# Kernel tuning notes

Measured on AMD Instinct MI355X. Metric: run time of the kernel, lower is better.

## Reference

```python
import jax, jax.numpy as jnp
import numpy as np

H, C = 8, 32          # heads, per-head channels (h_feats)
NEG_SLOPE = 0.2


def setup_inputs() -> dict:
    key = jax.random.key(0)
    ks = jax.random.split(key, 9)
    N, E, F_IN, F_E = 50000, 800000, 128, 16
    x = jax.random.normal(ks[0], (N, F_IN), jnp.float32)
    edge_index = jax.random.randint(ks[1], (2, E), 0, N, jnp.int64)
    edge_attr = jax.random.normal(ks[2], (E, F_E), jnp.float32)
    s = 1.0 / np.sqrt(F_IN)
    W = jax.random.normal(ks[3], (H * C, F_IN), jnp.float32) * s
    W_edge = jax.random.normal(ks[4], (H * C, F_E), jnp.float32) * (1.0 / np.sqrt(F_E))
    att_src = jax.random.normal(ks[5], (H, C), jnp.float32) * (1.0 / np.sqrt(C))
    att_dst = jax.random.normal(ks[6], (H, C), jnp.float32) * (1.0 / np.sqrt(C))
    att_edge = jax.random.normal(ks[7], (H, C), jnp.float32) * (1.0 / np.sqrt(C))
    bias = jnp.zeros((C,), jnp.float32)
    return {"x": x, "edge_index": edge_index, "edge_attr": edge_attr,
            "W": W, "W_edge": W_edge, "att_src": att_src, "att_dst": att_dst,
            "att_edge": att_edge, "bias": bias}


def reference(x, edge_index, edge_attr, W, W_edge, att_src, att_dst, att_edge, bias):
    N = x.shape[0]
    src, dst = edge_index[0], edge_index[1]

    # --- add self loops, edge_attr fill_value='mean' (per-dst mean of incoming attrs) ---
    deg = jax.ops.segment_sum(jnp.ones_like(dst, dtype=edge_attr.dtype), dst, num_segments=N)
    loop_attr = jax.ops.segment_sum(edge_attr, dst, num_segments=N) / jnp.maximum(deg, 1.0)[:, None]
    loop = jnp.arange(N, dtype=src.dtype)
    src = jnp.concatenate([src, loop])
    dst = jnp.concatenate([dst, loop])
    ea = jnp.concatenate([edge_attr, loop_attr], axis=0)  # [E+N, F_e]

    # --- node projection and per-node attention terms ---
    xh = (x @ W.T).reshape(N, H, C)                      # [N,H,C]
    a_src = jnp.einsum('nhc,hc->nh', xh, att_src)        # [N,H]
    a_dst = jnp.einsum('nhc,hc->nh', xh, att_dst)        # [N,H]

    # edge attention folded: (lin_edge(e).view(E,H,C) * att_edge).sum(-1) == e @ M
    M = jnp.einsum('hcf,hc->fh', W_edge.reshape(H, C, -1), att_edge)  # [F_e,H]
    a_edge = ea @ M                                      # [E+N,H]

    alpha = a_src[src] + a_dst[dst] + a_edge             # [E+N,H]
    alpha = jnp.where(alpha >= 0, alpha, NEG_SLOPE * alpha)

    # --- scatter-softmax over edges grouped by dst node ---
    amax = jax.ops.segment_max(alpha, dst, num_segments=N)  # every node has a self loop
    ex = jnp.exp(alpha - amax[dst])
    denom = jax.ops.segment_sum(ex, dst, num_segments=N)
    att = ex / denom[dst]                                # [E+N,H]

    # --- weighted message scatter-sum ---
    msg = xh[src] * att[..., None]                       # [E+N,H,C]
    out = jax.ops.segment_sum(msg, dst, num_segments=N)  # [N,H,C]
    return out.mean(axis=1) + bias                       # concat=False -> head mean
```

## Files before the change

### kernel.cpp

```cpp
#include <hip/hip_runtime.h>
#include <math.h>

#define H 8
#define C 32
#define HC 256
#define FE 16
#define FIN 128
#define NEG_SLOPE 0.2f

typedef __attribute__((ext_vector_type(8))) short bf16x8;
typedef __attribute__((ext_vector_type(4))) float f32x4;

__device__ __forceinline__ unsigned short f2bf(float f) {
  unsigned int u = __float_as_uint(f);
  unsigned int lsb = (u >> 16) & 1u;
  u += 0x7fffu + lsb;
  return (unsigned short)(u >> 16);
}
__device__ __forceinline__ float bf2f(unsigned short s) {
  return __uint_as_float(((unsigned int)s) << 16);
}

__device__ __forceinline__ void split8(const float* v, bf16x8& hi, bf16x8& lo) {
#pragma unroll
  for (int i = 0; i < 8; ++i) {
    unsigned int u = __float_as_uint(v[i]);
    unsigned int hu = u & 0xffff0000u;
    float r = v[i] - __uint_as_float(hu);
    hi[i] = (short)(hu >> 16);
    lo[i] = (short)f2bf(r);
  }
}

__global__ __launch_bounds__(256) void k_wsplit(const float* __restrict__ W,
                                                unsigned short* __restrict__ Whi,
                                                unsigned short* __restrict__ Wlo) {
  int i = blockIdx.x * 256 + threadIdx.x;
  float v = W[i];
  unsigned int u = __float_as_uint(v);
  unsigned int hu = u & 0xffff0000u;
  Whi[i] = (unsigned short)(hu >> 16);
  Wlo[i] = f2bf(v - __uint_as_float(hu)) , (unsigned short)0;
}

__global__ __launch_bounds__(256) void k_wsplit2(const float* __restrict__ W,
                                                 unsigned short* __restrict__ Whi,
                                                 unsigned short* __restrict__ Wlo) {
  int i = blockIdx.x * 256 + threadIdx.x;
  float v = W[i];
  unsigned int u = __float_as_uint(v);
  unsigned int hu = u & 0xffff0000u;
  Whi[i] = (unsigned short)(hu >> 16);
  Wlo[i] = f2bf(v - __uint_as_float(hu));
}

__global__ __launch_bounds__(256) void k_xh(const float* __restrict__ x,
                                            const unsigned short* __restrict__ Whi,
                                            const unsigned short* __restrict__ Wlo,
                                            const float* __restrict__ att_src,
                                            const float* __restrict__ att_dst,
                                            unsigned short* __restrict__ xhb,
                                            float* __restrict__ a_src,
                                            float* __restrict__ a_dst, int N) {
  int t = threadIdx.x;
  int w = t >> 6, lane = t & 63;
  int n15 = lane & 15, q = lane >> 4;
  int nodeBase = blockIdx.x * 128 + w * 32;
  int chBase = blockIdx.y * 128;

  f32x4 acc[8][2];
#pragma unroll
  for (int mt = 0; mt < 8; ++mt)
#pragma unroll
    for (int nt = 0; nt < 2; ++nt) acc[mt][nt] = (f32x4)(0.f);

  for (int ks = 0; ks < 4; ++ks) {
    int kOff = ks * 32 + q * 8;
    bf16x8 Bhi[2], Blo[2];
#pragma unroll
    for (int nt = 0; nt < 2; ++nt) {
      int node = nodeBase + nt * 16 + n15;
      int rn = (node < N) ? node : (N - 1);
      const float* px = &x[(size_t)rn * FIN + kOff];
      float vb[8];
      *(float4*)&vb[0] = *(const float4*)px;
      *(float4*)&vb[4] = *(const float4*)(px + 4);
      split8(vb, Bhi[nt], Blo[nt]);
    }
#pragma unroll
    for (int mt = 0; mt < 8; ++mt) {
      int widx = ((chBase + mt * 16 + n15) << 7) + kOff;
      bf16x8 Ahi = *(const bf16x8*)&Whi[widx];
      bf16x8 Alo = *(const bf16x8*)&Wlo[widx];
#pragma unroll
      for (int nt = 0; nt < 2; ++nt) {
        acc[mt][nt] = __builtin_amdgcn_mfma_f32_16x16x32_bf16(Ahi, Bhi[nt], acc[mt][nt], 0, 0, 0);
        acc[mt][nt] = __builtin_amdgcn_mfma_f32_16x16x32_bf16(Ahi, Blo[nt], acc[mt][nt], 0, 0, 0);
        acc[mt][nt] = __builtin_amdgcn_mfma_f32_16x16x32_bf16(Alo, Bhi[nt], acc[mt][nt], 0, 0, 0);
      }
    }
  }

  float ps[2][4] = {{0.f,0.f,0.f,0.f},{0.f,0.f,0.f,0.f}};
  float pd[2][4] = {{0.f,0.f,0.f,0.f},{0.f,0.f,0.f,0.f}};
#pragma unroll
  for (int mt = 0; mt < 8; ++mt) {
    int hl = mt >> 1;
#pragma unroll
    for (int r = 0; r < 4; ++r) {
      int ch = chBase + mt * 16 + q * 4 + r;
      float as_c = att_src[ch], ad_c = att_dst[ch];
#pragma unroll
      for (int nt = 0; nt < 2; ++nt) {
        float val = acc[mt][nt][r];
        ps[nt][hl] = fmaf(val, as_c, ps[nt][hl]);
        pd[nt][hl] = fmaf(val, ad_c, pd[nt][hl]);
      }
    }
#pragma unroll
    for (int nt = 0; nt < 2; ++nt) {
      int node = nodeBase + nt * 16 + n15;
      if (node < N) {
        ushort4 us;
        us.x = f2bf(acc[mt][nt][0]); us.y = f2bf(acc[mt][nt][1]);
        us.z = f2bf(acc[mt][nt][2]); us.w = f2bf(acc[mt][nt][3]);
        *(ushort4*)&xhb[(size_t)node * HC + chBase + mt * 16 + q * 4] = us;
      }
    }
  }
#pragma unroll
  for (int nt = 0; nt < 2; ++nt)
#pragma unroll
    for (int hl = 0; hl < 4; ++hl) {
      ps[nt][hl] += __shfl_xor(ps[nt][hl], 16, 64);
      ps[nt][hl] += __shfl_xor(ps[nt][hl], 32, 64);
      pd[nt][hl] += __shfl_xor(pd[nt][hl], 16, 64);
      pd[nt][hl] += __shfl_xor(pd[nt][hl], 32, 64);
    }
  if (q == 0) {
#pragma unroll
    for (int nt = 0; nt < 2; ++nt) {
      int node = nodeBase + nt * 16 + n15;
      if (node < N) {
        *(float4*)&a_src[node * H + blockIdx.y * 4] = make_float4(ps[nt][0], ps[nt][1], ps[nt][2], ps[nt][3]);
        *(float4*)&a_dst[node * H + blockIdx.y * 4] = make_float4(pd[nt][0], pd[nt][1], pd[nt][2], pd[nt][3]);
      }
    }
  }
}

__global__ __launch_bounds__(256) void k_deg(const int* __restrict__ ei,
                                             int* __restrict__ deg,
                                             int* __restrict__ rank, int E) {
  int e = blockIdx.x * 256 + threadIdx.x;
  if (e < E) rank[e] = atomicAdd(&deg[ei[E + e]], 1);
}

__global__ __launch_bounds__(256) void k_scan1(const int* __restrict__ deg,
                                               int* __restrict__ bsum, int N) {
  int t = threadIdx.x;
  int i = blockIdx.x * 256 + t;
  int v = (i < N) ? deg[i] : 0;
#pragma unroll
  for (int m = 1; m < 64; m <<= 1) v += __shfl_xor(v, m, 64);
  __shared__ int wsum[4];
  if ((t & 63) == 0) wsum[t >> 6] = v;
  __syncthreads();
  if (t == 0) bsum[blockIdx.x] = wsum[0] + wsum[1] + wsum[2] + wsum[3];
}

__global__ __launch_bounds__(256) void k_scan2(const int* __restrict__ bsum,
                                               int* __restrict__ boff, int nb) {
  __shared__ int buf[256];
  int t = threadIdx.x;
  int v = (t < nb) ? bsum[t] : 0;
  buf[t] = v;
  __syncthreads();
  for (int off = 1; off < 256; off <<= 1) {
    int y = (t >= off) ? buf[t - off] : 0;
    __syncthreads();
    buf[t] += y;
    __syncthreads();
  }
  if (t < nb) boff[t] = buf[t] - v;
}

__global__ __launch_bounds__(256) void k_scan3(const int* __restrict__ deg,
                                               const int* __restrict__ boff,
                                               int* __restrict__ rowptr, int N, int E) {
  __shared__ int buf[256];
  int t = threadIdx.x;
  int i = blockIdx.x * 256 + t;
  int v = (i < N) ? deg[i] : 0;
  buf[t] = v;
  __syncthreads();
  for (int off = 1; off < 256; off <<= 1) {
    int y = (t >= off) ? buf[t - off] : 0;
    __syncthreads();
    buf[t] += y;
    __syncthreads();
  }
  if (i < N) rowptr[i] = boff[blockIdx.x] + buf[t] - v;
  if (i == 0) rowptr[N] = E;
}

__global__ __launch_bounds__(256) void k_edge_scatter(const int* __restrict__ ei,
                                                      const float* __restrict__ ea,
                                                      const float* __restrict__ W_edge,
                                                      const float* __restrict__ att_edge,
                                                      const int* __restrict__ rowptr,
                                                      const int* __restrict__ rank,
                                                      unsigned short* __restrict__ recs, int E) {
  __shared__ float Ms[FE * H];
  int t = threadIdx.x;
  if (t < FE * H) {
    int f = t >> 3, h = t & 7;
    float acc = 0.f;
#pragma unroll
    for (int c = 0; c < C; ++c)
      acc += W_edge[(h * C + c) * FE + f] * att_edge[h * C + c];
    Ms[f * H + h] = acc;
  }
  __syncthreads();
  int e = blockIdx.x * 256 + t;
  if (e >= E) return;
  int s = ei[e], d = ei[E + e];
  const float4* p = (const float4*)&ea[(size_t)e * FE];
  float4 v0 = p[0], v1 = p[1], v2 = p[2], v3 = p[3];
  float eav[FE] = {v0.x, v0.y, v0.z, v0.w, v1.x, v1.y, v1.z, v1.w,
                   v2.x, v2.y, v2.z, v2.w, v3.x, v3.y, v3.z, v3.w};
  float o[H];
#pragma unroll
  for (int h = 0; h < H; ++h) {
    float acc = 0.f;
#pragma unroll
    for (int f = 0; f < FE; ++f) acc += eav[f] * Ms[f * H + h];
    o[h] = acc;
  }
  int pos = rowptr[d] + rank[e];
  uint4 pk;
  pk.x = (unsigned int)f2bf(o[0]) | ((unsigned int)f2bf(o[1]) << 16);
  pk.y = (unsigned int)f2bf(o[2]) | ((unsigned int)f2bf(o[3]) << 16);
  pk.z = (unsigned int)f2bf(o[4]) | ((unsigned int)f2bf(o[5]) << 16);
  pk.w = (unsigned int)f2bf(o[6]) | ((unsigned int)f2bf(o[7]) << 16);
  uint4 hv; hv.x = (unsigned int)s; hv.y = 0; hv.z = 0; hv.w = 0;
  unsigned short* rp = &recs[(size_t)pos * 16];
  *(uint4*)rp = pk;
  *(uint4*)(rp + 8) = hv;
}

__global__ __launch_bounds__(256) void k_node(const unsigned short* __restrict__ xhb,
                                              const float* __restrict__ a_src,
                                              const float* __restrict__ a_dst,
                                              const unsigned short* __restrict__ recs,
                                              const int* __restrict__ rowptr,
                                              const float* __restrict__ bias,
                                              float* __restrict__ out, int N) {
  __shared__ float wlds[4][512];
  __shared__ int   slds[4][64];
  int wv = threadIdx.x >> 6;
  int lane = threadIdx.x & 63;
  int n = blockIdx.x * 4 + wv;
  if (n >= N) return;
  int start = rowptr[n];
  int deg = rowptr[n + 1] - start;
  int h = lane & 7, esub = lane >> 3;
  float adst = a_dst[n * H + h];
  float asrc = a_src[n * H + h];

  float pmax = -1e30f, psum = 0.f;
  float a0, a1, a2, a3, a4, a5, a6, a7;
#define PH1(IT, AV)                                                          \
  {                                                                          \
    int j = IT * 8 + esub;                                                   \
    float al = -1e30f;                                                       \
    if (j < deg) {                                                           \
      int b = (start + j) * 16;                                              \
      float ae = bf2f(recs[b + h]);                                          \
      int src = *(const int*)&recs[b + 8];                                   \
      if (h == 0) slds[wv][j] = src;                                         \
      psum += ae;                                                            \
      al = a_src[src * H + h] + adst + ae;                                   \
      al = (al >= 0.f) ? al : NEG_SLOPE * al;                                \
      pmax = fmaxf(pmax, al);                                                \
    }                                                                        \
    AV = al;                                                                 \
  }
  PH1(0, a0) PH1(1, a1) PH1(2, a2) PH1(3, a3)
  PH1(4, a4) PH1(5, a5) PH1(6, a6) PH1(7, a7)
#undef PH1
  for (int j0 = 64; j0 < deg; j0 += 8) {
    int j = j0 + esub;
    if (j < deg) {
      int b = (start + j) * 16;
      float ae = bf2f(recs[b + h]);
      int src = *(const int*)&recs[b + 8];
      psum += ae;
      float al = a_src[src * H + h] + adst + ae;
      al = (al >= 0.f) ? al : NEG_SLOPE * al;
      pmax = fmaxf(pmax, al);
    }
  }
#pragma unroll
  for (int m = 8; m <= 32; m <<= 1) {
    pmax = fmaxf(pmax, __shfl_xor(pmax, m, 64));
    psum += __shfl_xor(psum, m, 64);
  }
  float aself = asrc + adst + psum / fmaxf((float)deg, 1.f);
  aself = (aself >= 0.f) ? aself : NEG_SLOPE * aself;
  float amax = fmaxf(pmax, aself);

  float den = 0.f;
#define PH2(IT, AV)                                                          \
  {                                                                          \
    int j = IT * 8 + esub;                                                   \
    if (j < deg) {                                                           \
      float wj = __expf(AV - amax);                                          \
      den += wj;                                                             \
      wlds[wv][j * 8 + h] = wj;                                              \
    }                                                                        \
  }
  PH2(0, a0) PH2(1, a1) PH2(2, a2) PH2(3, a3)
  PH2(4, a4) PH2(5, a5) PH2(6, a6) PH2(7, a7)
#undef PH2
  for (int j0 = 64; j0 < deg; j0 += 8) {
    int j = j0 + esub;
    if (j < deg) {
      int b = (start + j) * 16;
      float ae = bf2f(recs[b + h]);
      int src = *(const int*)&recs[b + 8];
      float al = a_src[src * H + h] + adst + ae;
      al = (al >= 0.f) ? al : NEG_SLOPE * al;
      den += __expf(al - amax);
    }
  }
#pragma unroll
  for (int m = 8; m <= 32; m <<= 1) den += __shfl_xor(den, m, 64);
  float wself = __expf(aself - amax);
  float inv = 1.f / (den + wself);

  int hc = lane >> 3;
  float inv_c  = __shfl(inv, hc, 64);
  float ws_c   = __shfl(wself, hc, 64);
  float amax_c = __shfl(amax, hc, 64);
  float adst_c = __shfl(adst, hc, 64);
  float accx, accy, accz, accw;
  {
    const uint2* px = (const uint2*)(xhb + (((unsigned)n) << 8));
    uint2 u = px[lane];
    accx = ws_c * __uint_as_float(u.x << 16);
    accy = ws_c * __uint_as_float(u.x & 0xffff0000u);
    accz = ws_c * __uint_as_float(u.y << 16);
    accw = ws_c * __uint_as_float(u.y & 0xffff0000u);
  }
  int dlim = (deg < 64) ? deg : 64;
#pragma unroll 2
  for (int j = 0; j < dlim; ++j) {
    float wj = wlds[wv][j * 8 + hc];
    int src = slds[wv][j];
    const uint2* p = (const uint2*)(xhb + (((unsigned)src) << 8));
    uint2 v = p[lane];
    accx = fmaf(__uint_as_float(v.x << 16), wj, accx);
    accy = fmaf(__uint_as_float(v.x & 0xffff0000u), wj, accy);
    accz = fmaf(__uint_as_float(v.y << 16), wj, accz);
    accw = fmaf(__uint_as_float(v.y & 0xffff0000u), wj, accw);
  }
  for (int j = 64; j < deg; ++j) {
    int b = (start + j) * 16;
    float ae = bf2f(recs[b + hc]);
    int src = *(const int*)&recs[b + 8];
    float al = a_src[src * H + hc] + adst_c + ae;
    al = (al >= 0.f) ? al : NEG_SLOPE * al;
    float wj = __expf(al - amax_c);
    const uint2* p = (const uint2*)(xhb + (((unsigned)src) << 8));
    uint2 v = p[lane];
    accx = fmaf(__uint_as_float(v.x << 16), wj, accx);
    accy = fmaf(__uint_as_float(v.x & 0xffff0000u), wj, accy);
    accz = fmaf(__uint_as_float(v.y << 16), wj, accz);
    accw = fmaf(__uint_as_float(v.y & 0xffff0000u), wj, accw);
  }
  accx *= inv_c; accy *= inv_c; accz *= inv_c; accw *= inv_c;

#pragma unroll
  for (int m = 8; m <= 32; m <<= 1) {
    accx += __shfl_xor(accx, m, 64);
    accy += __shfl_xor(accy, m, 64);
    accz += __shfl_xor(accz, m, 64);
    accw += __shfl_xor(accw, m, 64);
  }
  if (lane < 8) {
    float4 b = ((const float4*)bias)[lane];
    float4 o;
    o.x = accx * 0.125f + b.x;
    o.y = accy * 0.125f + b.y;
    o.z = accz * 0.125f + b.z;
    o.w = accw * 0.125f + b.w;
    ((float4*)&out[(size_t)n * C])[lane] = o;
  }
}

extern "C" void kernel_launch(void* const* d_in, const int* in_sizes, int n_in,
                              void* d_out, int out_size, void* d_ws, size_t ws_size,
                              hipStream_t stream) {
  const float* x        = (const float*)d_in[0];
  const int*   ei       = (const int*)d_in[1];
  const float* ea       = (const float*)d_in[2];
  const float* W        = (const float*)d_in[3];
  const float* W_edge   = (const float*)d_in[4];
  const float* att_src  = (const float*)d_in[5];
  const float* att_dst  = (const float*)d_in[6];
  const float* att_edge = (const float*)d_in[7];
  const float* bias     = (const float*)d_in[8];
  float* out = (float*)d_out;

  int N = in_sizes[0] / FIN;
  int E = in_sizes[1] / 2;
  int nb = (N + 255) / 256;

  char* ws = (char*)d_ws;
  auto take = [&](size_t bytes) {
    char* p = ws;
    ws += (bytes + 255) & ~(size_t)255;
    return p;
  };
  unsigned short* xhb    = (unsigned short*)take((size_t)N * HC * 2);
  float*          a_src  = (float*)take((size_t)N * H * 4);
  float*          a_dst  = (float*)take((size_t)N * H * 4);
  unsigned short* recs   = (unsigned short*)take((size_t)E * 32);
  unsigned short* Whi    = (unsigned short*)take((size_t)HC * FIN * 2);
  unsigned short* Wlo    = (unsigned short*)take((size_t)HC * FIN * 2);
  int*            deg    = (int*)take((size_t)N * 4);
  int*            rowptr = (int*)take((size_t)(N + 1) * 4);
  int*            rank   = (int*)take((size_t)E * 4);
  int*            bsum   = (int*)take((size_t)nb * 4);
  int*            boff   = (int*)take((size_t)nb * 4);

  hipMemsetAsync(deg, 0, (size_t)N * 4, stream);
  k_wsplit2<<<(HC * FIN) / 256, 256, 0, stream>>>(W, Whi, Wlo);
  k_deg<<<(E + 255) / 256, 256, 0, stream>>>(ei, deg, rank, E);
  k_xh<<<dim3((N + 127) / 128, 2), 256, 0, stream>>>(x, Whi, Wlo, att_src, att_dst, xhb, a_src, a_dst, N);
  k_scan1<<<nb, 256, 0, stream>>>(deg, bsum, N);
  k_scan2<<<1, 256, 0, stream>>>(bsum, boff, nb);
  k_scan3<<<nb, 256, 0, stream>>>(deg, boff, rowptr, N, E);
  k_edge_scatter<<<(E + 255) / 256, 256, 0, stream>>>(ei, ea, W_edge, att_edge, rowptr, rank, recs, E);
  k_node<<<(N + 3) / 4, 256, 0, stream>>>(xhb, a_src, a_dst, recs, rowptr, bias, out, N);
}
```

Baseline: 307.0 us.

## Batch edge gathers in k_node and fold W split into k_deg

The per-node kernel now issues all record loads for the first 64 edges up front, then all a_src gathers, before doing the softmax maths. The weighted-sum loop is software-pipelined so that eight neighbour feature rows are prefetched while the previous eight are accumulated. This is meant to raise memory-level parallelism and hide gather latency. The separate W hi/lo split kernel is merged into the degree-count kernel to save one launch, at the cost of more registers in k_node.

```diff
diff --git a/kernel.cpp b/kernel.cpp
--- a/kernel.cpp
+++ b/kernel.cpp
@@ -30,28 +30,6 @@
     hi[i] = (short)(hu >> 16);
     lo[i] = (short)f2bf(r);
   }
-}
-
-__global__ __launch_bounds__(256) void k_wsplit(const float* __restrict__ W,
-                                                unsigned short* __restrict__ Whi,
-                                                unsigned short* __restrict__ Wlo) {
-  int i = blockIdx.x * 256 + threadIdx.x;
-  float v = W[i];
-  unsigned int u = __float_as_uint(v);
-  unsigned int hu = u & 0xffff0000u;
-  Whi[i] = (unsigned short)(hu >> 16);
-  Wlo[i] = f2bf(v - __uint_as_float(hu)) , (unsigned short)0;
-}
-
-__global__ __launch_bounds__(256) void k_wsplit2(const float* __restrict__ W,
-                                                 unsigned short* __restrict__ Whi,
-                                                 unsigned short* __restrict__ Wlo) {
-  int i = blockIdx.x * 256 + threadIdx.x;
-  float v = W[i];
-  unsigned int u = __float_as_uint(v);
-  unsigned int hu = u & 0xffff0000u;
-  Whi[i] = (unsigned short)(hu >> 16);
-  Wlo[i] = f2bf(v - __uint_as_float(hu));
 }
 
 __global__ __launch_bounds__(256) void k_xh(const float* __restrict__ x,
@@ -151,8 +129,18 @@
 
 __global__ __launch_bounds__(256) void k_deg(const int* __restrict__ ei,
                                              int* __restrict__ deg,
-                                             int* __restrict__ rank, int E) {
+                                             int* __restrict__ rank,
+                                             const float* __restrict__ W,
+                                             unsigned short* __restrict__ Whi,
+                                             unsigned short* __restrict__ Wlo, int E) {
   int e = blockIdx.x * 256 + threadIdx.x;
+  if (e < HC * FIN) {
+    float v = W[e];
+    unsigned int u = __float_as_uint(v);
+    unsigned int hu = u & 0xffff0000u;
+    Whi[e] = (unsigned short)(hu >> 16);
+    Wlo[e] = f2bf(v - __uint_as_float(hu));
+  }
   if (e < E) rank[e] = atomicAdd(&deg[ei[E + e]], 1);
 }
 
@@ -264,41 +252,59 @@
   if (n >= N) return;
   int start = rowptr[n];
   int deg = rowptr[n + 1] - start;
+  int jmax = (deg < 64) ? deg : 64;
   int h = lane & 7, esub = lane >> 3;
   float adst = a_dst[n * H + h];
   float asrc = a_src[n * H + h];
 
+  float ae[8]; int sr[8];
+#pragma unroll
+  for (int it = 0; it < 8; ++it) {
+    int j = it * 8 + esub;
+    ae[it] = 0.f; sr[it] = 0;
+    if (j < jmax) {
+      const unsigned short* rp = &recs[(size_t)(start + j) * 16];
+      ae[it] = bf2f(rp[h]);
+      sr[it] = *(const int*)(rp + 8);
+    }
+  }
+  float asg[8];
+#pragma unroll
+  for (int it = 0; it < 8; ++it) {
+    int j = it * 8 + esub;
+    asg[it] = (j < jmax) ? a_src[sr[it] * H + h] : 0.f;
+  }
+  if (h == 0) {
+#pragma unroll
+    for (int it = 0; it < 8; ++it) {
+      int j = it * 8 + esub;
+      if (j < jmax) slds[wv][j] = sr[it];
+    }
+  }
+  float al[8];
   float pmax = -1e30f, psum = 0.f;
-  float a0, a1, a2, a3, a4, a5, a6, a7;
-#define PH1(IT, AV)                                                          \
-  {                                                                          \
-    int j = IT * 8 + esub;                                                   \
-    float al = -1e30f;                                                       \
-    if (j < deg) {                                                           \
-      int b = (start + j) * 16;                                              \
-      float ae = bf2f(recs[b + h]);                                          \
-      int src = *(const int*)&recs[b + 8];                                   \
-      if (h == 0) slds[wv][j] = src;                                         \
-      psum += ae;                                                            \
-      al = a_src[src * H + h] + adst + ae;                                   \
-      al = (al >= 0.f) ? al : NEG_SLOPE * al;                                \
-      pmax = fmaxf(pmax, al);                                                \
-    }                                                                        \
-    AV = al;                                                                 \
-  }
-  PH1(0, a0) PH1(1, a1) PH1(2, a2) PH1(3, a3)
-  PH1(4, a4) PH1(5, a5) PH1(6, a6) PH1(7, a7)
-#undef PH1
+#pragma unroll
+  for (int it = 0; it < 8; ++it) {
+    int j = it * 8 + esub;
+    float a = -1e30f;
+    if (j < jmax) {
+      psum += ae[it];
+      a = asg[it] + adst + ae[it];
+      a = (a >= 0.f) ? a : NEG_SLOPE * a;
+      pmax = fmaxf(pmax, a);
+    }
+    al[it] = a;
+  }
   for (int j0 = 64; j0 < deg; j0 += 8) {
     int j = j0 + esub;
     if (j < deg) {
-      int b = (start + j) * 16;
-      float ae = bf2f(recs[b + h]);
-      int src = *(const int*)&recs[b + 8];
-      psum += ae;
-      float al = a_src[src * H + h] + adst + ae;
-      al = (al >= 0.f) ? al : NEG_SLOPE * al;
-      pmax = fmaxf(pmax, al);
+      const unsigned short* rp = &recs[(size_t)(start + j) * 16];
+      float aev = bf2f(rp[h]);
+      int src = *(const int*)(rp + 8);
+      psum += aev;
+      float a = a_src[src * H + h] + adst + aev;
+      a = (a >= 0.f) ? a : NEG_SLOPE * a;
+      pmax = fmaxf(pmax, a);
     }
   }
 #pragma unroll
@@ -311,27 +317,24 @@
   float amax = fmaxf(pmax, aself);
 
   float den = 0.f;
-#define PH2(IT, AV)                                                          \
-  {                                                                          \
-    int j = IT * 8 + esub;                                                   \
-    if (j < deg) {                                                           \
-      float wj = __expf(AV - amax);                                          \
-      den += wj;                                                             \
-      wlds[wv][j * 8 + h] = wj;                                              \
-    }                                                                        \
-  }
-  PH2(0, a0) PH2(1, a1) PH2(2, a2) PH2(3, a3)
-  PH2(4, a4) PH2(5, a5) PH2(6, a6) PH2(7, a7)
-#undef PH2
+#pragma unroll
+  for (int it = 0; it < 8; ++it) {
+    int j = it * 8 + esub;
+    if (j < jmax) {
+      float wj = __expf(al[it] - amax);
+      den += wj;
+      wlds[wv][j * 8 + h] = wj;
+    }
+  }
   for (int j0 = 64; j0 < deg; j0 += 8) {
     int j = j0 + esub;
     if (j < deg) {
-      int b = (start + j) * 16;
-      float ae = bf2f(recs[b + h]);
-      int src = *(const int*)&recs[b + 8];
-      float al = a_src[src * H + h] + adst + ae;
-      al = (al >= 0.f) ? al : NEG_SLOPE * al;
-      den += __expf(al - amax);
+      const unsigned short* rp = &recs[(size_t)(start + j) * 16];
+      float aev = bf2f(rp[h]);
+      int src = *(const int*)(rp + 8);
+      float a = a_src[src * H + h] + adst + aev;
+      a = (a >= 0.f) ? a : NEG_SLOPE * a;
+      den += __expf(a - amax);
     }
   }
 #pragma unroll
@@ -346,34 +349,50 @@
   float adst_c = __shfl(adst, hc, 64);
   float accx, accy, accz, accw;
   {
-    const uint2* px = (const uint2*)(xhb + (((unsigned)n) << 8));
-    uint2 u = px[lane];
+    uint2 u = ((const uint2*)(xhb + (((size_t)n) << 8)))[lane];
     accx = ws_c * __uint_as_float(u.x << 16);
     accy = ws_c * __uint_as_float(u.x & 0xffff0000u);
     accz = ws_c * __uint_as_float(u.y << 16);
     accw = ws_c * __uint_as_float(u.y & 0xffff0000u);
   }
-  int dlim = (deg < 64) ? deg : 64;
-#pragma unroll 2
-  for (int j = 0; j < dlim; ++j) {
-    float wj = wlds[wv][j * 8 + hc];
-    int src = slds[wv][j];
-    const uint2* p = (const uint2*)(xhb + (((unsigned)src) << 8));
-    uint2 v = p[lane];
-    accx = fmaf(__uint_as_float(v.x << 16), wj, accx);
-    accy = fmaf(__uint_as_float(v.x & 0xffff0000u), wj, accy);
-    accz = fmaf(__uint_as_float(v.y << 16), wj, accz);
-    accw = fmaf(__uint_as_float(v.y & 0xffff0000u), wj, accw);
+  uint2 va[8]; float wa[8];
+#pragma unroll
+  for (int k = 0; k < 8; ++k) {
+    va[k] = make_uint2(0u, 0u); wa[k] = 0.f;
+    if (k < jmax) {
+      wa[k] = wlds[wv][k * 8 + hc];
+      va[k] = ((const uint2*)(xhb + (((size_t)slds[wv][k]) << 8)))[lane];
+    }
+  }
+  for (int j0 = 0; j0 < jmax; j0 += 8) {
+    uint2 vb[8]; float wb[8];
+#pragma unroll
+    for (int k = 0; k < 8; ++k) {
+      int jn = j0 + 8 + k;
+      vb[k] = make_uint2(0u, 0u); wb[k] = 0.f;
+      if (jn < jmax) {
+        wb[k] = wlds[wv][jn * 8 + hc];
+        vb[k] = ((const uint2*)(xhb + (((size_t)slds[wv][jn]) << 8)))[lane];
+      }
+    }
+#pragma unroll
+    for (int k = 0; k < 8; ++k) {
+      uint2 v = va[k]; float wj = wa[k];
+      accx = fmaf(__uint_as_float(v.x << 16), wj, accx);
+      accy = fmaf(__uint_as_float(v.x & 0xffff0000u), wj, accy);
+      accz = fmaf(__uint_as_float(v.y << 16), wj, accz);
+      accw = fmaf(__uint_as_float(v.y & 0xffff0000u), wj, accw);
+      va[k] = vb[k]; wa[k] = wb[k];
+    }
   }
   for (int j = 64; j < deg; ++j) {
-    int b = (start + j) * 16;
-    float ae = bf2f(recs[b + hc]);
-    int src = *(const int*)&recs[b + 8];
-    float al = a_src[src * H + hc] + adst_c + ae;
-    al = (al >= 0.f) ? al : NEG_SLOPE * al;
-    float wj = __expf(al - amax_c);
-    const uint2* p = (const uint2*)(xhb + (((unsigned)src) << 8));
-    uint2 v = p[lane];
+    const unsigned short* rp = &recs[(size_t)(start + j) * 16];
+    float aev = bf2f(rp[hc]);
+    int src = *(const int*)(rp + 8);
+    float a = a_src[src * H + hc] + adst_c + aev;
+    a = (a >= 0.f) ? a : NEG_SLOPE * a;
+    float wj = __expf(a - amax_c);
+    uint2 v = ((const uint2*)(xhb + (((size_t)src) << 8)))[lane];
     accx = fmaf(__uint_as_float(v.x << 16), wj, accx);
     accy = fmaf(__uint_as_float(v.x & 0xffff0000u), wj, accy);
     accz = fmaf(__uint_as_float(v.y << 16), wj, accz);
@@ -436,8 +455,7 @@
   int*            boff   = (int*)take((size_t)nb * 4);
 
   hipMemsetAsync(deg, 0, (size_t)N * 4, stream);
-  k_wsplit2<<<(HC * FIN) / 256, 256, 0, stream>>>(W, Whi, Wlo);
-  k_deg<<<(E + 255) / 256, 256, 0, stream>>>(ei, deg, rank, E);
+  k_deg<<<(E + 255) / 256, 256, 0, stream>>>(ei, deg, rank, W, Whi, Wlo, E);
   k_xh<<<dim3((N + 127) / 128, 2), 256, 0, stream>>>(x, Whi, Wlo, att_src, att_dst, xhb, a_src, a_dst, N);
   k_scan1<<<nb, 256, 0, stream>>>(deg, bsum, N);
   k_scan2<<<1, 256, 0, stream>>>(bsum, boff, nb);
```

New measurement: 317.0 us. +3.3%, slower.
